# Optimization experiments

Hardware: AMD Instinct MI355X
Metric: run time of the kernel (lower is better)

## Reference

```python
import jax, jax.numpy as jnp
import numpy as np

BETA = 5.5
ALPHA = 0.5

def _l2norm(x, eps=1e-12):
    # matches torch F.normalize(dim=-1): x / max(||x||, eps)
    n = jnp.sqrt(jnp.sum(x * x, axis=-1, keepdims=True))
    return x / jnp.maximum(n, eps)

def setup_inputs() -> dict:
    key = jax.random.key(0)
    k1, k2 = jax.random.split(key)
    query_features = jax.random.normal(k1, (4096, 512), dtype=jnp.float32)
    support_keys = jax.random.normal(k2, (16384, 512), dtype=jnp.float32)
    return {"query_features": query_features, "support_keys": support_keys}

def reference(query_features, support_keys):
    cache_keys = _l2norm(support_keys)              # (N, D)
    q = _l2norm(query_features)                     # (B, D)
    affinity = jnp.einsum('bd,nd->bn', q, cache_keys)   # (B, N) cosine sims
    affinity = jnp.exp(-BETA * (1.0 - affinity))
    retrieved = jnp.einsum('bn,nd->bd', affinity, cache_keys)  # (B, D)
    return query_features + ALPHA * retrieved
```

## Files before the change

### kernel.cpp

```cpp
#include <hip/hip_runtime.h>
#include <cstdint>
#include <cstddef>

#define BETA 5.5f
#define ALPHA 0.5f

constexpr int D   = 512;
constexpr int NB  = 4096;
constexpr int NK  = 16384;
constexpr int BQ  = 64;
constexpr int BN  = 64;
constexpr int NSPLIT = 4;
constexpr int NRANGE = NK / NSPLIT;
constexpr int CHUNKS = NRANGE / BN;
constexpr int KROW = D + 8;
constexpr int PROW = BN + 8;

typedef __attribute__((ext_vector_type(8)))  short    short8;
typedef __attribute__((ext_vector_type(4)))  float    floatx4;
typedef __attribute__((ext_vector_type(4)))  uint32_t uint4v;
typedef __attribute__((ext_vector_type(2)))  uint32_t uint2v;

__device__ inline uint32_t f2bf1(float f) {
  union { float f; uint32_t u; } v; v.f = f;
  return (v.u + 0x7FFFu + ((v.u >> 16) & 1u)) >> 16;
}
__device__ inline uint32_t pack2(float a, float b) {
  return f2bf1(a) | (f2bf1(b) << 16);
}

__device__ inline void load_lds16(const void* g, void* l) {
  __builtin_amdgcn_global_load_lds(
      (const __attribute__((address_space(1))) uint32_t*)g,
      (__attribute__((address_space(3))) uint32_t*)l, 16, 0, 0);
}

__global__ void norm_q_kernel(const float* __restrict__ q,
                              float* __restrict__ out,
                              unsigned short* __restrict__ Qn) {
  const int wave = threadIdx.x >> 6, lane = threadIdx.x & 63;
  const int row = blockIdx.x * 4 + wave;
  const float4* qr = (const float4*)(q + (size_t)row * D);
  float4 a = qr[lane * 2];
  float4 b = qr[lane * 2 + 1];
  float ss = a.x*a.x + a.y*a.y + a.z*a.z + a.w*a.w
           + b.x*b.x + b.y*b.y + b.z*b.z + b.w*b.w;
#pragma unroll
  for (int m = 32; m >= 1; m >>= 1) ss += __shfl_xor(ss, m, 64);
  const float sc = 1.0f / fmaxf(sqrtf(ss), 1e-12f);
  float4* orow = (float4*)(out + (size_t)row * D);
  orow[lane * 2]     = a;
  orow[lane * 2 + 1] = b;
  uint4v w;
  w.x = pack2(a.x*sc, a.y*sc); w.y = pack2(a.z*sc, a.w*sc);
  w.z = pack2(b.x*sc, b.y*sc); w.w = pack2(b.z*sc, b.w*sc);
  *(uint4v*)(Qn + (size_t)row * D + lane * 8) = w;
}

__global__ void norm_k_kernel(const float* __restrict__ k,
                              unsigned short* __restrict__ Kn,
                              unsigned short* __restrict__ KnT) {
  __shared__ unsigned short tile[64 * KROW];
  const int wave = threadIdx.x >> 6, lane = threadIdx.x & 63;
  const int n0 = blockIdx.x * 64;
#pragma unroll
  for (int i = 0; i < 4; ++i) {
    const int rl = wave * 4 + i;
    const int n  = n0 + rl;
    const float4* kr = (const float4*)(k + (size_t)n * D);
    float4 a = kr[lane * 2], b = kr[lane * 2 + 1];
    float ss = a.x*a.x + a.y*a.y + a.z*a.z + a.w*a.w
             + b.x*b.x + b.y*b.y + b.z*b.z + b.w*b.w;
#pragma unroll
    for (int m = 32; m >= 1; m >>= 1) ss += __shfl_xor(ss, m, 64);
    const float sc = 1.0f / fmaxf(sqrtf(ss), 1e-12f);
    uint4v w;
    w.x = pack2(a.x*sc, a.y*sc); w.y = pack2(a.z*sc, a.w*sc);
    w.z = pack2(b.x*sc, b.y*sc); w.w = pack2(b.z*sc, b.w*sc);
    *(uint4v*)(Kn + (size_t)n * D + lane * 8) = w;
    *(uint4v*)&tile[rl * KROW + lane * 8]     = w;
  }
  __syncthreads();
  const int dsub = threadIdx.x >> 3;
  const int nl   = (threadIdx.x & 7) * 8;
#pragma unroll
  for (int iter = 0; iter < 4; ++iter) {
    const int d = iter * 128 + dsub;
    uint4v w;
    w.x = (uint32_t)tile[(nl+0)*KROW + d] | ((uint32_t)tile[(nl+1)*KROW + d] << 16);
    w.y = (uint32_t)tile[(nl+2)*KROW + d] | ((uint32_t)tile[(nl+3)*KROW + d] << 16);
    w.z = (uint32_t)tile[(nl+4)*KROW + d] | ((uint32_t)tile[(nl+5)*KROW + d] << 16);
    w.w = (uint32_t)tile[(nl+6)*KROW + d] | ((uint32_t)tile[(nl+7)*KROW + d] << 16);
    *(uint4v*)(KnT + (size_t)d * NK + n0 + nl) = w;
  }
}

__global__ __launch_bounds__(512, 2) void fused_kernel(
    const unsigned short* __restrict__ Qn,
    const unsigned short* __restrict__ Kn,
    const unsigned short* __restrict__ KnT,
    float* __restrict__ out) {
  __shared__ unsigned short K_lds[2][BN * KROW];
  __shared__ unsigned short P_lds[2][BQ * PROW];

  const int tid  = threadIdx.x;
  const int wave = tid >> 6, lane = tid & 63;
  const int l15  = lane & 15, quad = lane >> 4;
  const int nsplit = blockIdx.x & (NSPLIT - 1);
  const int qtile  = blockIdx.x >> 2;
  const int q0     = qtile * BQ;
  const int nbase  = nsplit * NRANGE;
  const int tb = wave & 3, nh = wave >> 2;

  short8 qf[16];
  {
    const unsigned short* qrow = Qn + (size_t)(q0 + tb * 16 + l15) * D + quad * 8;
#pragma unroll
    for (int kb = 0; kb < 16; ++kb) qf[kb] = *(const short8*)(qrow + kb * 32);
  }

  floatx4 oacc[4][4] = {};
  short8 ktf[2][4];

  const unsigned short* ktrow = KnT + (size_t)(wave*64 + l15) * NK + nbase + quad*8;

  auto stage = [&](int ch, int buf) {
#pragma unroll
    for (int i = 0; i < 8; ++i) {
      const int row = wave * 8 + i;
      load_lds16(Kn + (size_t)(nbase + ch*BN + row) * D + lane * 8,
                 &K_lds[buf][row * KROW]);
    }
  };
  auto gemm1_half = [&](int buf, int kb0, floatx4& s0, floatx4& s1) {
#pragma unroll
    for (int kb = kb0; kb < kb0 + 8; ++kb) {
      short8 a0 = *(const short8*)&K_lds[buf][(nh*32 +      l15) * KROW + kb*32 + quad*8];
      short8 a1 = *(const short8*)&K_lds[buf][(nh*32 + 16 + l15) * KROW + kb*32 + quad*8];
      s0 = __builtin_amdgcn_mfma_f32_16x16x32_bf16(a0, qf[kb], s0, 0, 0, 0);
      s1 = __builtin_amdgcn_mfma_f32_16x16x32_bf16(a1, qf[kb], s1, 0, 0, 0);
    }
  };
  auto gemm2_half = [&](int buf, int kb2) {
    short8 pf[4];
#pragma unroll
    for (int tr = 0; tr < 4; ++tr)
      pf[tr] = *(const short8*)&P_lds[buf][(tr*16 + l15) * PROW + kb2*32 + quad*8];
#pragma unroll
    for (int td = 0; td < 4; ++td)
#pragma unroll
      for (int tr = 0; tr < 4; ++tr)
        oacc[tr][td] = __builtin_amdgcn_mfma_f32_16x16x32_bf16(
            pf[tr], ktf[kb2][td], oacc[tr][td], 0, 0, 0);
  };
  auto ktf_load = [&](int ch) {
#pragma unroll
    for (int kb2 = 0; kb2 < 2; ++kb2)
#pragma unroll
      for (int td = 0; td < 4; ++td)
        ktf[kb2][td] = *(const short8*)(ktrow + (size_t)td*16*NK + ch*BN + kb2*32);
  };
  auto exp_pw = [&](int buf, const floatx4& s0, const floatx4& s1) {
    const int prow = (tb * 16 + l15) * PROW;
    uint2v w0, w1;
    w0.x = pack2(__expf(BETA * (s0[0] - 1.f)), __expf(BETA * (s0[1] - 1.f)));
    w0.y = pack2(__expf(BETA * (s0[2] - 1.f)), __expf(BETA * (s0[3] - 1.f)));
    w1.x = pack2(__expf(BETA * (s1[0] - 1.f)), __expf(BETA * (s1[1] - 1.f)));
    w1.y = pack2(__expf(BETA * (s1[2] - 1.f)), __expf(BETA * (s1[3] - 1.f)));
    *(uint2v*)&P_lds[buf][prow + (nh*2 + 0) * 16 + quad * 4] = w0;
    *(uint2v*)&P_lds[buf][prow + (nh*2 + 1) * 16 + quad * 4] = w1;
  };

  stage(0, 0);
  ktf_load(0);
  __syncthreads();
  {
    stage(1, 1);
    floatx4 s0 = {}, s1 = {};
    gemm1_half(0, 0, s0, s1);
    gemm1_half(0, 8, s0, s1);
    exp_pw(0, s0, s1);
  }
  __syncthreads();

#pragma unroll 1
  for (int c = 0; c + 2 < CHUNKS; ++c) {
    const int cur = c & 1, nxt = cur ^ 1;
    stage(c + 2, cur);
    floatx4 s0 = {}, s1 = {};
    gemm2_half(cur, 0);
    gemm1_half(nxt, 0, s0, s1);
    gemm2_half(cur, 1);
    gemm1_half(nxt, 8, s0, s1);
    ktf_load(c + 1);
    exp_pw(nxt, s0, s1);
    __syncthreads();
  }
  {
    const int c = CHUNKS - 2, cur = c & 1, nxt = cur ^ 1;
    floatx4 s0 = {}, s1 = {};
    gemm2_half(cur, 0);
    gemm1_half(nxt, 0, s0, s1);
    gemm2_half(cur, 1);
    gemm1_half(nxt, 8, s0, s1);
    ktf_load(CHUNKS - 1);
    exp_pw(nxt, s0, s1);
    __syncthreads();
  }
  {
    const int cur = (CHUNKS - 1) & 1;
    gemm2_half(cur, 0);
    gemm2_half(cur, 1);
  }

  const int colbase = wave * 64 + l15;
#pragma unroll
  for (int tr = 0; tr < 4; ++tr)
#pragma unroll
    for (int td = 0; td < 4; ++td)
#pragma unroll
      for (int r = 0; r < 4; ++r)
        atomicAdd(out + (size_t)(q0 + tr*16 + quad*4 + r) * D + colbase + td*16,
                  ALPHA * oacc[tr][td][r]);
}

extern "C" void kernel_launch(void* const* d_in, const int* in_sizes, int n_in,
                              void* d_out, int out_size, void* d_ws, size_t ws_size,
                              hipStream_t stream) {
  (void)in_sizes; (void)n_in; (void)out_size; (void)ws_size;
  const float* q = (const float*)d_in[0];
  const float* k = (const float*)d_in[1];
  float* out = (float*)d_out;
  unsigned short* Qn  = (unsigned short*)d_ws;
  unsigned short* Kn  = Qn + (size_t)NB * D;
  unsigned short* KnT = Kn + (size_t)NK * D;

  hipLaunchKernelGGL(norm_q_kernel, dim3(NB / 4),  dim3(256),  0, stream, q, out, Qn);
  hipLaunchKernelGGL(norm_k_kernel, dim3(NK / 64), dim3(1024), 0, stream, k, Kn, KnT);
  hipLaunchKernelGGL(fused_kernel, dim3((NB / BQ) * NSPLIT), dim3(512), 0, stream,
                     Qn, Kn, KnT, out);
}
```

Before: 311.0 us.

## Warp-specialize fused kernel into score/exp producer and output-GEMM consumer waves

Splits the eight waves of each block into two roles. Waves 0-3 compute QK^T scores with 2x2 MFMA tiles and write the exp'd probabilities into LDS. Waves 4-7 load K^T fragments and accumulate P·K into 64x128 output tiles, then do the atomic adds. Before, every wave interleaved both GEMMs; the split is meant to give each role better register reuse and let the two GEMM phases overlap across waves. In exchange, consumer waves carry twice the accumulator registers (128 floats), which risks spills under launch_bounds(512,2), and the two roles may be unevenly loaded.

```diff
diff --git a/kernel.cpp b/kernel.cpp
--- a/kernel.cpp
+++ b/kernel.cpp
@@ -110,118 +110,128 @@
   const int qtile  = blockIdx.x >> 2;
   const int q0     = qtile * BQ;
   const int nbase  = nsplit * NRANGE;
-  const int tb = wave & 3, nh = wave >> 2;
-
-  short8 qf[16];
-  {
-    const unsigned short* qrow = Qn + (size_t)(q0 + tb * 16 + l15) * D + quad * 8;
-#pragma unroll
-    for (int kb = 0; kb < 16; ++kb) qf[kb] = *(const short8*)(qrow + kb * 32);
-  }
-
-  floatx4 oacc[4][4] = {};
-  short8 ktf[2][4];
-
-  const unsigned short* ktrow = KnT + (size_t)(wave*64 + l15) * NK + nbase + quad*8;
 
   auto stage = [&](int ch, int buf) {
 #pragma unroll
     for (int i = 0; i < 8; ++i) {
       const int row = wave * 8 + i;
-      load_lds16(Kn + (size_t)(nbase + ch*BN + row) * D + lane * 8,
+      load_lds16(Kn + (size_t)(nbase + ch * BN + row) * D + lane * 8,
                  &K_lds[buf][row * KROW]);
     }
   };
-  auto gemm1_half = [&](int buf, int kb0, floatx4& s0, floatx4& s1) {
-#pragma unroll
-    for (int kb = kb0; kb < kb0 + 8; ++kb) {
-      short8 a0 = *(const short8*)&K_lds[buf][(nh*32 +      l15) * KROW + kb*32 + quad*8];
-      short8 a1 = *(const short8*)&K_lds[buf][(nh*32 + 16 + l15) * KROW + kb*32 + quad*8];
-      s0 = __builtin_amdgcn_mfma_f32_16x16x32_bf16(a0, qf[kb], s0, 0, 0, 0);
-      s1 = __builtin_amdgcn_mfma_f32_16x16x32_bf16(a1, qf[kb], s1, 0, 0, 0);
-    }
-  };
-  auto gemm2_half = [&](int buf, int kb2) {
-    short8 pf[4];
+
+  if (wave < 4) {
+    const int qh = wave & 1, nh = wave >> 1;
+    short8 qf[2][16];
+    {
+      const unsigned short* qrow0 = Qn + (size_t)(q0 + qh * 32 + l15) * D + quad * 8;
+#pragma unroll
+      for (int qt = 0; qt < 2; ++qt)
+#pragma unroll
+        for (int kb = 0; kb < 16; ++kb)
+          qf[qt][kb] = *(const short8*)(qrow0 + (size_t)qt * 16 * D + kb * 32);
+    }
+
+    auto gemm1x = [&](int buf, int pbuf) {
+      floatx4 sacc[2][2] = {};
+#pragma unroll
+      for (int kb = 0; kb < 16; ++kb) {
+        short8 a0 = *(const short8*)&K_lds[buf][(nh*32 +      l15) * KROW + kb*32 + quad*8];
+        short8 a1 = *(const short8*)&K_lds[buf][(nh*32 + 16 + l15) * KROW + kb*32 + quad*8];
+        sacc[0][0] = __builtin_amdgcn_mfma_f32_16x16x32_bf16(a0, qf[0][kb], sacc[0][0], 0, 0, 0);
+        sacc[0][1] = __builtin_amdgcn_mfma_f32_16x16x32_bf16(a0, qf[1][kb], sacc[0][1], 0, 0, 0);
+        sacc[1][0] = __builtin_amdgcn_mfma_f32_16x16x32_bf16(a1, qf[0][kb], sacc[1][0], 0, 0, 0);
+        sacc[1][1] = __builtin_amdgcn_mfma_f32_16x16x32_bf16(a1, qf[1][kb], sacc[1][1], 0, 0, 0);
+      }
+#pragma unroll
+      for (int qt = 0; qt < 2; ++qt)
+#pragma unroll
+        for (int nt = 0; nt < 2; ++nt) {
+          const floatx4 s = sacc[nt][qt];
+          uint2v w;
+          w.x = pack2(__expf(BETA * (s[0] - 1.f)), __expf(BETA * (s[1] - 1.f)));
+          w.y = pack2(__expf(BETA * (s[2] - 1.f)), __expf(BETA * (s[3] - 1.f)));
+          *(uint2v*)&P_lds[pbuf][(qh*32 + qt*16 + l15) * PROW + nh*32 + nt*16 + quad*4] = w;
+        }
+    };
+
+    stage(0, 0);
+    __syncthreads();
+    stage(1, 1);
+    gemm1x(0, 0);
+    __syncthreads();
+
+#pragma unroll 1
+    for (int c = 0; c + 2 < CHUNKS; ++c) {
+      const int cur = c & 1, nxt = cur ^ 1;
+      stage(c + 2, cur);
+      gemm1x(nxt, nxt);
+      __syncthreads();
+    }
+    gemm1x((CHUNKS - 1) & 1, (CHUNKS - 1) & 1);
+    __syncthreads();
+  } else {
+    const int w4 = wave - 4;
+    floatx4 oacc[4][8] = {};
+    short8 ktf[2][8];
+    const unsigned short* ktbase = KnT + (size_t)(w4 * 128 + l15) * NK + nbase + quad * 8;
+
+    auto ktf_half = [&](int ch, int kb2) {
+#pragma unroll
+      for (int td = 0; td < 8; ++td)
+        ktf[kb2][td] = *(const short8*)(ktbase + (size_t)td * 16 * NK + ch * BN + kb2 * 32);
+    };
+    auto gemm2_half = [&](int pbuf, int kb2) {
+      short8 pf[4];
+#pragma unroll
+      for (int tr = 0; tr < 4; ++tr)
+        pf[tr] = *(const short8*)&P_lds[pbuf][(tr*16 + l15) * PROW + kb2*32 + quad*8];
+#pragma unroll
+      for (int td = 0; td < 8; ++td)
+#pragma unroll
+        for (int tr = 0; tr < 4; ++tr)
+          oacc[tr][td] = __builtin_amdgcn_mfma_f32_16x16x32_bf16(
+              pf[tr], ktf[kb2][td], oacc[tr][td], 0, 0, 0);
+    };
+
+    stage(0, 0);
+    __syncthreads();
+    stage(1, 1);
+    ktf_half(0, 0); ktf_half(0, 1);
+    __syncthreads();
+
+#pragma unroll 1
+    for (int c = 0; c + 2 < CHUNKS; ++c) {
+      const int cur = c & 1;
+      stage(c + 2, cur);
+      gemm2_half(cur, 0);
+      ktf_half(c + 1, 0);
+      gemm2_half(cur, 1);
+      ktf_half(c + 1, 1);
+      __syncthreads();
+    }
+    {
+      const int cur = (CHUNKS - 2) & 1;
+      gemm2_half(cur, 0); ktf_half(CHUNKS - 1, 0);
+      gemm2_half(cur, 1); ktf_half(CHUNKS - 1, 1);
+      __syncthreads();
+    }
+    {
+      const int cur = (CHUNKS - 1) & 1;
+      gemm2_half(cur, 0);
+      gemm2_half(cur, 1);
+    }
+
+    const int colbase = w4 * 128 + l15;
 #pragma unroll
     for (int tr = 0; tr < 4; ++tr)
-      pf[tr] = *(const short8*)&P_lds[buf][(tr*16 + l15) * PROW + kb2*32 + quad*8];
-#pragma unroll
-    for (int td = 0; td < 4; ++td)
-#pragma unroll
-      for (int tr = 0; tr < 4; ++tr)
-        oacc[tr][td] = __builtin_amdgcn_mfma_f32_16x16x32_bf16(
-            pf[tr], ktf[kb2][td], oacc[tr][td], 0, 0, 0);
-  };
-  auto ktf_load = [&](int ch) {
-#pragma unroll
-    for (int kb2 = 0; kb2 < 2; ++kb2)
-#pragma unroll
-      for (int td = 0; td < 4; ++td)
-        ktf[kb2][td] = *(const short8*)(ktrow + (size_t)td*16*NK + ch*BN + kb2*32);
-  };
-  auto exp_pw = [&](int buf, const floatx4& s0, const floatx4& s1) {
-    const int prow = (tb * 16 + l15) * PROW;
-    uint2v w0, w1;
-    w0.x = pack2(__expf(BETA * (s0[0] - 1.f)), __expf(BETA * (s0[1] - 1.f)));
-    w0.y = pack2(__expf(BETA * (s0[2] - 1.f)), __expf(BETA * (s0[3] - 1.f)));
-    w1.x = pack2(__expf(BETA * (s1[0] - 1.f)), __expf(BETA * (s1[1] - 1.f)));
-    w1.y = pack2(__expf(BETA * (s1[2] - 1.f)), __expf(BETA * (s1[3] - 1.f)));
-    *(uint2v*)&P_lds[buf][prow + (nh*2 + 0) * 16 + quad * 4] = w0;
-    *(uint2v*)&P_lds[buf][prow + (nh*2 + 1) * 16 + quad * 4] = w1;
-  };
-
-  stage(0, 0);
-  ktf_load(0);
-  __syncthreads();
-  {
-    stage(1, 1);
-    floatx4 s0 = {}, s1 = {};
-    gemm1_half(0, 0, s0, s1);
-    gemm1_half(0, 8, s0, s1);
-    exp_pw(0, s0, s1);
+#pragma unroll
+      for (int td = 0; td < 8; ++td)
+#pragma unroll
+        for (int r = 0; r < 4; ++r)
+          atomicAdd(out + (size_t)(q0 + tr*16 + quad*4 + r) * D + colbase + td*16,
+                    ALPHA * oacc[tr][td][r]);
   }
-  __syncthreads();
-
-#pragma unroll 1
-  for (int c = 0; c + 2 < CHUNKS; ++c) {
-    const int cur = c & 1, nxt = cur ^ 1;
-    stage(c + 2, cur);
-    floatx4 s0 = {}, s1 = {};
-    gemm2_half(cur, 0);
-    gemm1_half(nxt, 0, s0, s1);
-    gemm2_half(cur, 1);
-    gemm1_half(nxt, 8, s0, s1);
-    ktf_load(c + 1);
-    exp_pw(nxt, s0, s1);
-    __syncthreads();
-  }
-  {
-    const int c = CHUNKS - 2, cur = c & 1, nxt = cur ^ 1;
-    floatx4 s0 = {}, s1 = {};
-    gemm2_half(cur, 0);
-    gemm1_half(nxt, 0, s0, s1);
-    gemm2_half(cur, 1);
-    gemm1_half(nxt, 8, s0, s1);
-    ktf_load(CHUNKS - 1);
-    exp_pw(nxt, s0, s1);
-    __syncthreads();
-  }
-  {
-    const int cur = (CHUNKS - 1) & 1;
-    gemm2_half(cur, 0);
-    gemm2_half(cur, 1);
-  }
-
-  const int colbase = wave * 64 + l15;
-#pragma unroll
-  for (int tr = 0; tr < 4; ++tr)
-#pragma unroll
-    for (int td = 0; td < 4; ++td)
-#pragma unroll
-      for (int r = 0; r < 4; ++r)
-        atomicAdd(out + (size_t)(q0 + tr*16 + quad*4 + r) * D + colbase + td*16,
-                  ALPHA * oacc[tr][td][r]);
 }
 
 extern "C" void kernel_launch(void* const* d_in, const int* in_sizes, int n_in,
```

Result: slower. 322.8 us (+3.8%).

## Ping-pong MFMA phases with barriers, priority and explicit waitcnts in fused loop

Applied to the files above, without the earlier changes.

Splits the fused kernel's main loop into small phases. LDS fragment reads are issued before barrier-bracketed MFMA bursts that run at raised s_setprio, with sched_barrier fences to stop the compiler reordering them. The K-transpose global fragment loads are split into halves and interleaved across the phases. __syncthreads is replaced by explicit s_waitcnt vmcnt/lgkmcnt plus s_barrier, so in-flight global loads can stay outstanding. The aim is to interleave memory and MFMA work across the two resident blocks' waves, at the cost of many more barriers per chunk and fragile hand-managed wait counts.

```diff
diff --git a/kernel.cpp b/kernel.cpp
--- a/kernel.cpp
+++ b/kernel.cpp
@@ -132,33 +132,37 @@
                  &K_lds[buf][row * KROW]);
     }
   };
-  auto gemm1_half = [&](int buf, int kb0, floatx4& s0, floatx4& s1) {
-#pragma unroll
-    for (int kb = kb0; kb < kb0 + 8; ++kb) {
-      short8 a0 = *(const short8*)&K_lds[buf][(nh*32 +      l15) * KROW + kb*32 + quad*8];
-      short8 a1 = *(const short8*)&K_lds[buf][(nh*32 + 16 + l15) * KROW + kb*32 + quad*8];
-      s0 = __builtin_amdgcn_mfma_f32_16x16x32_bf16(a0, qf[kb], s0, 0, 0, 0);
-      s1 = __builtin_amdgcn_mfma_f32_16x16x32_bf16(a1, qf[kb], s1, 0, 0, 0);
-    }
-  };
-  auto gemm2_half = [&](int buf, int kb2) {
-    short8 pf[4];
+  auto ktf_load_h = [&](int ch, int kb2) {
+#pragma unroll
+    for (int td = 0; td < 4; ++td)
+      ktf[kb2][td] = *(const short8*)(ktrow + (size_t)td*16*NK + ch*BN + kb2*32);
+  };
+  auto pf_read = [&](int pbuf, int kb2, short8* pf) {
 #pragma unroll
     for (int tr = 0; tr < 4; ++tr)
-      pf[tr] = *(const short8*)&P_lds[buf][(tr*16 + l15) * PROW + kb2*32 + quad*8];
+      pf[tr] = *(const short8*)&P_lds[pbuf][(tr*16 + l15) * PROW + kb2*32 + quad*8];
+  };
+  auto gemm2_mfma = [&](const short8* pf, const short8* kt) {
 #pragma unroll
     for (int td = 0; td < 4; ++td)
 #pragma unroll
       for (int tr = 0; tr < 4; ++tr)
         oacc[tr][td] = __builtin_amdgcn_mfma_f32_16x16x32_bf16(
-            pf[tr], ktf[kb2][td], oacc[tr][td], 0, 0, 0);
-  };
-  auto ktf_load = [&](int ch) {
-#pragma unroll
-    for (int kb2 = 0; kb2 < 2; ++kb2)
-#pragma unroll
-      for (int td = 0; td < 4; ++td)
-        ktf[kb2][td] = *(const short8*)(ktrow + (size_t)td*16*NK + ch*BN + kb2*32);
+            pf[tr], kt[td], oacc[tr][td], 0, 0, 0);
+  };
+  auto a_read4 = [&](int buf, int kb0, short8* af) {
+#pragma unroll
+    for (int i = 0; i < 4; ++i) {
+      af[2*i]   = *(const short8*)&K_lds[buf][(nh*32 +      l15) * KROW + (kb0+i)*32 + quad*8];
+      af[2*i+1] = *(const short8*)&K_lds[buf][(nh*32 + 16 + l15) * KROW + (kb0+i)*32 + quad*8];
+    }
+  };
+  auto gemm1_mfma4 = [&](const short8* af, int kb0, floatx4& s0, floatx4& s1) {
+#pragma unroll
+    for (int i = 0; i < 4; ++i) {
+      s0 = __builtin_amdgcn_mfma_f32_16x16x32_bf16(af[2*i],   qf[kb0+i], s0, 0, 0, 0);
+      s1 = __builtin_amdgcn_mfma_f32_16x16x32_bf16(af[2*i+1], qf[kb0+i], s1, 0, 0, 0);
+    }
   };
   auto exp_pw = [&](int buf, const floatx4& s0, const floatx4& s1) {
     const int prow = (tb * 16 + l15) * PROW;
@@ -170,47 +174,101 @@
     *(uint2v*)&P_lds[buf][prow + (nh*2 + 0) * 16 + quad * 4] = w0;
     *(uint2v*)&P_lds[buf][prow + (nh*2 + 1) * 16 + quad * 4] = w1;
   };
+  auto ph_begin = [&]() {
+    asm volatile("s_barrier" ::: "memory");
+    asm volatile("s_waitcnt lgkmcnt(0)" ::: "memory");
+    __builtin_amdgcn_sched_barrier(0);
+    __builtin_amdgcn_s_setprio(1);
+  };
+  auto ph_end = [&]() {
+    __builtin_amdgcn_s_setprio(0);
+    __builtin_amdgcn_sched_barrier(0);
+    asm volatile("s_barrier" ::: "memory");
+  };
 
   stage(0, 0);
-  ktf_load(0);
-  __syncthreads();
+  ktf_load_h(0, 0); ktf_load_h(0, 1);
+  asm volatile("s_waitcnt vmcnt(8)" ::: "memory");
+  asm volatile("s_barrier" ::: "memory");
   {
     stage(1, 1);
-    floatx4 s0 = {}, s1 = {};
-    gemm1_half(0, 0, s0, s1);
-    gemm1_half(0, 8, s0, s1);
+    floatx4 s0 = {0.f,0.f,0.f,0.f}, s1 = {0.f,0.f,0.f,0.f};
+    short8 af[8];
+#pragma unroll
+    for (int g = 0; g < 4; ++g) {
+      a_read4(0, g*4, af);
+      gemm1_mfma4(af, g*4, s0, s1);
+    }
     exp_pw(0, s0, s1);
   }
-  __syncthreads();
+  asm volatile("s_waitcnt vmcnt(0) lgkmcnt(0)" ::: "memory");
+  asm volatile("s_barrier" ::: "memory");
 
 #pragma unroll 1
   for (int c = 0; c + 2 < CHUNKS; ++c) {
     const int cur = c & 1, nxt = cur ^ 1;
+    floatx4 s0 = {0.f,0.f,0.f,0.f}, s1 = {0.f,0.f,0.f,0.f};
+    short8 pf[4], af[8];
     stage(c + 2, cur);
-    floatx4 s0 = {}, s1 = {};
-    gemm2_half(cur, 0);
-    gemm1_half(nxt, 0, s0, s1);
-    gemm2_half(cur, 1);
-    gemm1_half(nxt, 8, s0, s1);
-    ktf_load(c + 1);
+    pf_read(cur, 0, pf);
+    ph_begin(); gemm2_mfma(pf, ktf[0]); ph_end();
+    a_read4(nxt, 0, af);
+    ph_begin(); gemm1_mfma4(af, 0, s0, s1); ph_end();
+    a_read4(nxt, 4, af);
+    ph_begin(); gemm1_mfma4(af, 4, s0, s1); ph_end();
+    pf_read(cur, 1, pf);
+    ktf_load_h(c + 1, 0);
+    ph_begin(); gemm2_mfma(pf, ktf[1]); ph_end();
+    a_read4(nxt, 8, af);
+    ktf_load_h(c + 1, 1);
+    ph_begin(); gemm1_mfma4(af, 8, s0, s1); ph_end();
+    a_read4(nxt, 12, af);
+    asm volatile("s_barrier" ::: "memory");
+    asm volatile("s_waitcnt lgkmcnt(0)" ::: "memory");
+    __builtin_amdgcn_sched_barrier(0);
+    __builtin_amdgcn_s_setprio(1);
+    gemm1_mfma4(af, 12, s0, s1);
+    __builtin_amdgcn_s_setprio(0);
+    __builtin_amdgcn_sched_barrier(0);
     exp_pw(nxt, s0, s1);
-    __syncthreads();
+    asm volatile("s_waitcnt vmcnt(8) lgkmcnt(0)" ::: "memory");
+    asm volatile("s_barrier" ::: "memory");
   }
   {
     const int c = CHUNKS - 2, cur = c & 1, nxt = cur ^ 1;
-    floatx4 s0 = {}, s1 = {};
-    gemm2_half(cur, 0);
-    gemm1_half(nxt, 0, s0, s1);
-    gemm2_half(cur, 1);
-    gemm1_half(nxt, 8, s0, s1);
-    ktf_load(CHUNKS - 1);
+    floatx4 s0 = {0.f,0.f,0.f,0.f}, s1 = {0.f,0.f,0.f,0.f};
+    short8 pf[4], af[8];
+    pf_read(cur, 0, pf);
+    ph_begin(); gemm2_mfma(pf, ktf[0]); ph_end();
+    a_read4(nxt, 0, af);
+    ph_begin(); gemm1_mfma4(af, 0, s0, s1); ph_end();
+    a_read4(nxt, 4, af);
+    ph_begin(); gemm1_mfma4(af, 4, s0, s1); ph_end();
+    pf_read(cur, 1, pf);
+    ktf_load_h(CHUNKS - 1, 0);
+    ph_begin(); gemm2_mfma(pf, ktf[1]); ph_end();
+    a_read4(nxt, 8, af);
+    ktf_load_h(CHUNKS - 1, 1);
+    ph_begin(); gemm1_mfma4(af, 8, s0, s1); ph_end();
+    a_read4(nxt, 12, af);
+    asm volatile("s_barrier" ::: "memory");
+    asm volatile("s_waitcnt lgkmcnt(0)" ::: "memory");
+    __builtin_amdgcn_sched_barrier(0);
+    __builtin_amdgcn_s_setprio(1);
+    gemm1_mfma4(af, 12, s0, s1);
+    __builtin_amdgcn_s_setprio(0);
+    __builtin_amdgcn_sched_barrier(0);
     exp_pw(nxt, s0, s1);
-    __syncthreads();
+    asm volatile("s_waitcnt lgkmcnt(0)" ::: "memory");
+    asm volatile("s_barrier" ::: "memory");
   }
   {
     const int cur = (CHUNKS - 1) & 1;
-    gemm2_half(cur, 0);
-    gemm2_half(cur, 1);
+    short8 pf[4];
+    pf_read(cur, 0, pf);
+    gemm2_mfma(pf, ktf[0]);
+    pf_read(cur, 1, pf);
+    gemm2_mfma(pf, ktf[1]);
   }
 
   const int colbase = wave * 64 + l15;
```

New measurement: 334.7 us. 1.08x slower.
